# Kernel optimization log

Hardware: AMD Instinct MI355X
Metric: run time of the kernel (lower is better)

## Reference

```python
import jax, jax.numpy as jnp
import numpy as np

B = 131072
H_GAS = 8
H_EXT = 16
# gas order and net counts, total 99 tiny MLPs
GAS_SIZES = [23, 29, 13, 9, 3, 9, 13]  # h2o, h2o_sq, o3, co2, n2o, ch4, u
N_NETS = 29

# index maps taken verbatim from the 29 tau_gases assignment lines
H2O_ROWS = np.arange(23)
H2O_IDX = np.array([0,1,2,3,4,5,6,3,4,9,10,11,12,13,14,15,16,17,18,19,20,21,22])
O3_ROWS = np.array([0,1,2,17,18,19,20,21,22,25,26,27,28])
CO2_ROWS = np.array([0,1,2,5,6,9,10,13,14])
N2O_ROWS = np.array([0,1,2])
CH4_ROWS = np.array([0,1,2,3,4,7,8,11,12])
U_ROWS = np.array([0,1,2,15,16,17,18,19,20,21,22,27,28])


def setup_inputs() -> dict:
    key = jax.random.key(0)
    ks = jax.random.split(key, 23)
    f = jnp.float32
    inp = {
        'temp': jax.random.normal(ks[0], (B, 1), f),
        'pressure': jax.random.normal(ks[1], (B, 1), f),
        'comp_h2o': jax.random.uniform(ks[2], (B, 1), f),
        'comp_h2o_sq': jax.random.uniform(ks[3], (B, 1), f),
        'comp_o3': jax.random.uniform(ks[4], (B, 1), f),
        'comp_co2': jax.random.uniform(ks[5], (B, 1), f),
        'comp_n2o': jax.random.uniform(ks[6], (B, 1), f),
        'comp_ch4': jax.random.uniform(ks[7], (B, 1), f),
        'comp_u': jax.random.uniform(ks[8], (B, 1), f),
        'lwp': jax.random.uniform(ks[9], (B, 1), f, minval=0.05, maxval=1.0),
        'iwp': jax.random.uniform(ks[10], (B, 1), f, minval=0.05, maxval=1.0),
        'mu': jax.random.uniform(ks[11], (B, 1), f, minval=0.1, maxval=1.0),
        'mu_bar': jax.random.uniform(ks[12], (B, 1), f, minval=0.1, maxval=1.0),
        'gas_W1': jax.random.normal(ks[13], (99, 2, H_GAS), f) * 0.5,
        'gas_b1': jax.random.normal(ks[14], (99, H_GAS), f) * 0.1,
        'gas_W2': jax.random.normal(ks[15], (99, H_GAS, 1), f) * 0.5,
        'gas_b2': jax.random.uniform(ks[16], (99, 1), f, minval=0.05, maxval=0.5),
        'lw_w': jax.random.uniform(ks[17], (N_NETS, 1), f, minval=0.05, maxval=1.0),
        'iw_w': jax.random.uniform(ks[18], (N_NETS, 1), f, minval=0.05, maxval=1.0),
        'ext_W1': jax.random.normal(ks[19], (N_NETS, 4, H_EXT), f) * 0.5,
        'ext_b1': jax.random.normal(ks[20], (N_NETS, H_EXT), f) * 0.1,
        'ext_W2': jax.random.normal(ks[21], (N_NETS, H_EXT, 3), f) * 0.5,
        'ext_b2': jax.random.normal(ks[22], (N_NETS, 3), f) * 0.1,
    }
    return inp


def reference(temp, pressure, comp_h2o, comp_h2o_sq, comp_o3, comp_co2, comp_n2o,
              comp_ch4, comp_u, lwp, iwp, mu, mu_bar,
              gas_W1, gas_b1, gas_W2, gas_b2, lw_w, iw_w,
              ext_W1, ext_b1, ext_W2, ext_b2):
    b = temp.shape[0]
    X = jnp.concatenate([temp, pressure], axis=-1)              # [B,2]
    # all 99 per-gas tiny MLPs in one batched pass
    h = jax.nn.elu(jnp.einsum('bi,nih->nbh', X, gas_W1) + gas_b1[:, None, :])
    ke = jax.nn.relu(jnp.einsum('nbh,nho->nbo', h, gas_W2) + gas_b2[:, None, :])[..., 0]  # [99,B]
    comps = [comp_h2o, comp_h2o_sq, comp_o3, comp_co2, comp_n2o, comp_ch4, comp_u]
    comp_all = jnp.concatenate(
        [jnp.broadcast_to(c[:, 0][None, :], (n, b)) for c, n in zip(comps, GAS_SIZES)], axis=0)
    tau_all = ke * comp_all                                      # [99,B]
    h2o    = tau_all[0:23]
    h2o_sq = tau_all[23:52]
    o3     = tau_all[52:65]
    co2    = tau_all[65:74]
    n2o    = tau_all[74:77]
    ch4    = tau_all[77:86]
    u      = tau_all[86:99]
    # scatter-combine into the 29 spectral channels
    tau_g = h2o_sq                                               # every row has h2o_sq[k]
    tau_g = tau_g.at[H2O_ROWS].add(h2o[H2O_IDX])
    tau_g = tau_g.at[O3_ROWS].add(o3)
    tau_g = tau_g.at[CO2_ROWS].add(co2)
    tau_g = tau_g.at[N2O_ROWS].add(n2o)
    tau_g = tau_g.at[CH4_ROWS].add(ch4)
    tau_g = tau_g.at[U_ROWS].add(u)
    tau_lw = lw_w * lwp[:, 0][None, :]                           # [29,B]
    tau_iw = iw_w * iwp[:, 0][None, :]
    tau_total = tau_g + tau_lw + tau_iw
    in1 = tau_lw / tau_total
    in2 = tau_iw / tau_total
    mu_v, mub_v = mu[:, 0], mu_bar[:, 0]
    in3_dir = tau_total / mu_v[None, :]
    in3_dif = tau_total / mub_v[None, :]

    def ext(i1, i2, i3, m):
        Xe = jnp.stack([i1, i2, i3, jnp.broadcast_to(m[None, :], i1.shape)], axis=-1)  # [29,B,4]
        he = jax.nn.elu(jnp.einsum('nbi,nih->nbh', Xe, ext_W1) + ext_b1[:, None, :])
        return jax.nn.relu(jnp.einsum('nbh,nho->nbo', he, ext_W2) + ext_b2[:, None, :])

    e_direct = jax.nn.softmax(ext(in1, in2, in3_dir, mu_v), axis=-1)   # [29,B,3]
    e_diffuse = jax.nn.softmax(ext(in1, in2, in3_dif, mub_v), axis=-1)
    t_direct = jnp.exp(-in3_dir)
    t_diffuse = jnp.exp(-in3_dif)
    return (t_direct, t_diffuse, e_direct, e_diffuse)
```

## Files before the change

### kernel.cpp

```cpp
#include <hip/hip_runtime.h>
#include <math.h>

#define TPB 256
#define EPT 2

typedef float v2f __attribute__((ext_vector_type(2)));

#define VFMA(a, b, c) __builtin_elementwise_fma((a), (b), (c))
#define VMAX(a, b) __builtin_elementwise_max((a), (b))
#define LOG2E 1.4426950408889634f

struct f3 { float a, b, c; };

static __device__ __forceinline__ v2f sp(float s) { return (v2f){s, s}; }

static __device__ __forceinline__ float fexp2(float x) {
#if __has_builtin(__builtin_amdgcn_exp2f)
    return __builtin_amdgcn_exp2f(x);
#else
    return __expf(x * 0.6931471805599453f);
#endif
}

static __device__ __forceinline__ float fast_rcp(float x) {
    return __builtin_amdgcn_rcpf(x);
}

static __device__ __forceinline__ v2f elu2(v2f h) {
    v2f t = h * LOG2E;
    v2f e = {fexp2(t.x), fexp2(t.y)};
    e = e - 1.0f;
    return (v2f){h.x > 0.f ? h.x : e.x, h.y > 0.f ? h.y : e.y};
}

static __device__ const unsigned char NETS[29][8] = {
    {  0, 23,  52,  65,  74,  77,  86, 255},
    {  1, 24,  53,  66,  75,  78,  87, 255},
    {  2, 25,  54,  67,  76,  79,  88, 255},
    {  3, 26, 255, 255, 255,  80, 255, 255},
    {  4, 27, 255, 255, 255,  81, 255, 255},
    {  5, 28, 255,  68, 255, 255, 255, 255},
    {  6, 29, 255,  69, 255, 255, 255, 255},
    {  3, 30, 255, 255, 255,  82, 255, 255},
    {  4, 31, 255, 255, 255,  83, 255, 255},
    {  9, 32, 255,  70, 255, 255, 255, 255},
    { 10, 33, 255,  71, 255, 255, 255, 255},
    { 11, 34, 255, 255, 255,  84, 255, 255},
    { 12, 35, 255, 255, 255,  85, 255, 255},
    { 13, 36, 255,  72, 255, 255, 255, 255},
    { 14, 37, 255,  73, 255, 255, 255, 255},
    { 15, 38, 255, 255, 255, 255,  89, 255},
    { 16, 39, 255, 255, 255, 255,  90, 255},
    { 17, 40,  55, 255, 255, 255,  91, 255},
    { 18, 41,  56, 255, 255, 255,  92, 255},
    { 19, 42,  57, 255, 255, 255,  93, 255},
    { 20, 43,  58, 255, 255, 255,  94, 255},
    { 21, 44,  59, 255, 255, 255,  95, 255},
    { 22, 45,  60, 255, 255, 255,  96, 255},
    {255, 46, 255, 255, 255, 255, 255, 255},
    {255, 47, 255, 255, 255, 255, 255, 255},
    {255, 48,  61, 255, 255, 255, 255, 255},
    {255, 49,  62, 255, 255, 255, 255, 255},
    {255, 50,  63, 255, 255, 255,  97, 255},
    {255, 51,  64, 255, 255, 255,  98, 255}};

static __device__ __forceinline__ void softmax3_v2(v2f o0, v2f o1, v2f o2,
                                                   v2f& r0, v2f& r1, v2f& r2) {
    o0 = VMAX(o0, sp(0.f));
    o1 = VMAX(o1, sp(0.f));
    o2 = VMAX(o2, sp(0.f));
    v2f mx = VMAX(o0, VMAX(o1, o2));
    v2f nm = mx * (-LOG2E);
    v2f a0 = VFMA(o0, sp(LOG2E), nm);
    v2f a1 = VFMA(o1, sp(LOG2E), nm);
    v2f a2 = VFMA(o2, sp(LOG2E), nm);
    v2f e0 = {fexp2(a0.x), fexp2(a0.y)};
    v2f e1 = {fexp2(a1.x), fexp2(a1.y)};
    v2f e2 = {fexp2(a2.x), fexp2(a2.y)};
    v2f ssum = e0 + e1 + e2;
    v2f rs = {fast_rcp(ssum.x), fast_rcp(ssum.y)};
    r0 = e0 * rs; r1 = e1 * rs; r2 = e2 * rs;
}

template <bool GUARD>
__global__ __launch_bounds__(TPB, 5) void atm_kernel(
    const float* __restrict__ temp,
    const float* __restrict__ pressure,
    const float* __restrict__ c_h2o,
    const float* __restrict__ c_h2o_sq,
    const float* __restrict__ c_o3,
    const float* __restrict__ c_co2,
    const float* __restrict__ c_n2o,
    const float* __restrict__ c_ch4,
    const float* __restrict__ c_u,
    const float* __restrict__ lwp,
    const float* __restrict__ iwp,
    const float* __restrict__ mu,
    const float* __restrict__ mu_bar,
    const float* __restrict__ gW1,
    const float* __restrict__ gb1,
    const float* __restrict__ gW2,
    const float* __restrict__ gb2,
    const float* __restrict__ lw_w,
    const float* __restrict__ iw_w,
    const float* __restrict__ eW1,
    const float* __restrict__ eb1,
    const float* __restrict__ eW2,
    const float* __restrict__ eb2,
    float* __restrict__ out,
    int Bn)
{
    const int r = blockIdx.x;
    const int bA = blockIdx.y * (TPB * EPT) + threadIdx.x;
    if (GUARD && bA >= Bn) return;
    const int bB = bA + TPB;
    bool vB = true;
    int bBl = bB;
    if (GUARD) { vB = (bB < Bn); bBl = vB ? bB : bA; }

    const v2f t2  = {temp[bA],     temp[bBl]};
    const v2f p2  = {pressure[bA], pressure[bBl]};
    const v2f lwp2 = {lwp[bA],    lwp[bBl]};
    const v2f iwp2 = {iwp[bA],    iwp[bBl]};
    const v2f mu2  = {mu[bA],     mu[bBl]};
    const v2f mb2  = {mu_bar[bA], mu_bar[bBl]};

    v2f tg = sp(0.f);
    #pragma unroll
    for (int s = 0; s < 7; ++s) {
        const int n = NETS[r][s];
        if (n != 255) {
            const float* cp =
                (s == 0) ? c_h2o    : (s == 1) ? c_h2o_sq :
                (s == 2) ? c_o3     : (s == 3) ? c_co2    :
                (s == 4) ? c_n2o    : (s == 5) ? c_ch4    : c_u;
            const v2f cs = {cp[bA], cp[bBl]};
            const float4* W1 = (const float4*)(gW1 + (n << 4));
            const float4 wt0 = W1[0], wt1 = W1[1];
            const float4 wp0 = W1[2], wp1 = W1[3];
            const float4* B1 = (const float4*)(gb1 + (n << 3));
            const float4 bb0 = B1[0], bb1 = B1[1];
            const float4* W2 = (const float4*)(gW2 + (n << 3));
            const float4 wo0 = W2[0], wo1 = W2[1];
            v2f acc = sp(gb2[n]);
#define GAS_H(WT, WP, BB, WO, K)                                            \
            { v2f h = VFMA(t2, sp((WT).K), VFMA(p2, sp((WP).K), sp((BB).K))); \
              h = elu2(h);                                                   \
              acc = VFMA(h, sp((WO).K), acc); }
            GAS_H(wt0, wp0, bb0, wo0, x)
            GAS_H(wt0, wp0, bb0, wo0, y)
            GAS_H(wt0, wp0, bb0, wo0, z)
            GAS_H(wt0, wp0, bb0, wo0, w)
            GAS_H(wt1, wp1, bb1, wo1, x)
            GAS_H(wt1, wp1, bb1, wo1, y)
            GAS_H(wt1, wp1, bb1, wo1, z)
            GAS_H(wt1, wp1, bb1, wo1, w)
#undef GAS_H
            acc = VMAX(acc, sp(0.f));
            tg = VFMA(acc, cs, tg);
        }
    }

    const float lwr = lw_w[r], iwr = iw_w[r];
    v2f tlw = lwp2 * lwr;
    v2f tiw = iwp2 * iwr;
    v2f tt = tg + tlw + tiw;
    v2f rtt = {fast_rcp(tt.x), fast_rcp(tt.y)};
    v2f in1 = tlw * rtt;
    v2f in2 = tiw * rtt;
    v2f rmu = {fast_rcp(mu2.x), fast_rcp(mu2.y)};
    v2f rmb = {fast_rcp(mb2.x), fast_rcp(mb2.y)};
    v2f i3d = tt * rmu;
    v2f i3f = tt * rmb;

    const int idxA = r * Bn + bA;
    {
        v2f ad = i3d * (-LOG2E);
        v2f af = i3f * (-LOG2E);
        out[idxA] = fexp2(ad.x);
        out[29 * Bn + idxA] = fexp2(af.x);
        if (vB) {
            out[idxA + TPB] = fexp2(ad.y);
            out[29 * Bn + idxA + TPB] = fexp2(af.y);
        }
    }

    const float* w1  = eW1 + (r << 6);
    const float* ebv = eb1 + (r << 4);
    const float* w2  = eW2 + r * 48;
    const float bo0 = eb2[r * 3 + 0];
    const float bo1 = eb2[r * 3 + 1];
    const float bo2 = eb2[r * 3 + 2];

    v2f d0 = sp(bo0), d1 = sp(bo1), d2 = sp(bo2);
    v2f f0 = sp(bo0), f1 = sp(bo1), f2 = sp(bo2);

    #pragma unroll
    for (int q = 0; q < 4; ++q) {
        const float4 wA4 = *(const float4*)(w1 + 4 * q);
        const float4 wB4 = *(const float4*)(w1 + 16 + 4 * q);
        const float4 wC4 = *(const float4*)(w1 + 32 + 4 * q);
        const float4 wD4 = *(const float4*)(w1 + 48 + 4 * q);
        const float4 bj4 = *(const float4*)(ebv + 4 * q);
        const float4 u0  = *(const float4*)(w2 + 12 * q);
        const float4 u1  = *(const float4*)(w2 + 12 * q + 4);
        const float4 u2  = *(const float4*)(w2 + 12 * q + 8);
#define EXT_H(K, W20, W21, W22)                                               \
        { v2f bs = VFMA(in1, sp((wA4).K), VFMA(in2, sp((wB4).K), sp((bj4).K))); \
          v2f hd = elu2(VFMA(i3d, sp((wC4).K), VFMA(mu2, sp((wD4).K), bs)));   \
          v2f hf = elu2(VFMA(i3f, sp((wC4).K), VFMA(mb2, sp((wD4).K), bs)));   \
          d0 = VFMA(hd, sp(W20), d0); d1 = VFMA(hd, sp(W21), d1);              \
          d2 = VFMA(hd, sp(W22), d2);                                          \
          f0 = VFMA(hf, sp(W20), f0); f1 = VFMA(hf, sp(W21), f1);              \
          f2 = VFMA(hf, sp(W22), f2); }
        EXT_H(x, u0.x, u0.y, u0.z)
        EXT_H(y, u0.w, u1.x, u1.y)
        EXT_H(z, u1.z, u1.w, u2.x)
        EXT_H(w, u2.y, u2.z, u2.w)
#undef EXT_H
    }

    v2f r0, r1, r2;
    softmax3_v2(d0, d1, d2, r0, r1, r2);
    f3* pdA = (f3*)(out + 58 * Bn) + idxA;
    pdA[0] = (f3){r0.x, r1.x, r2.x};
    if (vB) pdA[TPB] = (f3){r0.y, r1.y, r2.y};
    softmax3_v2(f0, f1, f2, r0, r1, r2);
    f3* pfA = (f3*)(out + 145 * Bn) + idxA;
    pfA[0] = (f3){r0.x, r1.x, r2.x};
    if (vB) pfA[TPB] = (f3){r0.y, r1.y, r2.y};
}

extern "C" void kernel_launch(void* const* d_in, const int* in_sizes, int n_in,
                              void* d_out, int out_size, void* d_ws, size_t ws_size,
                              hipStream_t stream) {
    const int Bn = in_sizes[0];
    const int span = TPB * EPT;
    dim3 grid(29, (Bn + span - 1) / span);
    if (Bn % span == 0) {
        atm_kernel<false><<<grid, TPB, 0, stream>>>(
            (const float*)d_in[0],  (const float*)d_in[1],  (const float*)d_in[2],
            (const float*)d_in[3],  (const float*)d_in[4],  (const float*)d_in[5],
            (const float*)d_in[6],  (const float*)d_in[7],  (const float*)d_in[8],
            (const float*)d_in[9],  (const float*)d_in[10], (const float*)d_in[11],
            (const float*)d_in[12], (const float*)d_in[13], (const float*)d_in[14],
            (const float*)d_in[15], (const float*)d_in[16], (const float*)d_in[17],
            (const float*)d_in[18], (const float*)d_in[19], (const float*)d_in[20],
            (const float*)d_in[21], (const float*)d_in[22],
            (float*)d_out, Bn);
    } else {
        atm_kernel<true><<<grid, TPB, 0, stream>>>(
            (const float*)d_in[0],  (const float*)d_in[1],  (const float*)d_in[2],
            (const float*)d_in[3],  (const float*)d_in[4],  (const float*)d_in[5],
            (const float*)d_in[6],  (const float*)d_in[7],  (const float*)d_in[8],
            (const float*)d_in[9],  (const float*)d_in[10], (const float*)d_in[11],
            (const float*)d_in[12], (const float*)d_in[13], (const float*)d_in[14],
            (const float*)d_in[15], (const float*)d_in[16], (const float*)d_in[17],
            (const float*)d_in[18], (const float*)d_in[19], (const float*)d_in[20],
            (const float*)d_in[21], (const float*)d_in[22],
            (float*)d_out, Bn);
    }
}
```

Measured before the change: 210.5 us.

## Add grid-stride persistent kernel and branchless ELU, pack pointers in struct

Replaces the 2D grid of 29×256 blocks with a 1D grid-stride kernel capped near 2048 blocks, each looping over (row, batch-tile) items, when the batch tile count is a power of two. ELU is rewritten branchlessly as max(h,0)+exp(min(h,0))-1. Launch bounds drop the minimum-blocks hint of 5, which may change register allocation and occupancy. Kernel arguments are packed into a struct.

```diff
diff --git a/kernel.cpp b/kernel.cpp
--- a/kernel.cpp
+++ b/kernel.cpp
@@ -8,9 +8,21 @@
 
 #define VFMA(a, b, c) __builtin_elementwise_fma((a), (b), (c))
 #define VMAX(a, b) __builtin_elementwise_max((a), (b))
+#define VMIN(a, b) __builtin_elementwise_min((a), (b))
 #define LOG2E 1.4426950408889634f
 
 struct f3 { float a, b, c; };
+
+struct Ptrs {
+    const float *temp, *pressure;
+    const float *c0, *c1, *c2, *c3, *c4, *c5, *c6;
+    const float *lwp, *iwp, *mu, *mub;
+    const float *gW1, *gb1, *gW2, *gb2;
+    const float *lww, *iww;
+    const float *eW1, *eb1, *eW2, *eb2;
+    float* out;
+    int Bn;
+};
 
 static __device__ __forceinline__ v2f sp(float s) { return (v2f){s, s}; }
 
@@ -27,10 +39,9 @@
 }
 
 static __device__ __forceinline__ v2f elu2(v2f h) {
-    v2f t = h * LOG2E;
+    v2f t = VMIN(h, sp(0.f)) * LOG2E;
     v2f e = {fexp2(t.x), fexp2(t.y)};
-    e = e - 1.0f;
-    return (v2f){h.x > 0.f ? h.x : e.x, h.y > 0.f ? h.y : e.y};
+    return VMAX(h, sp(0.f)) + e - 1.0f;
 }
 
 static __device__ const unsigned char NETS[29][8] = {
@@ -83,47 +94,16 @@
 }
 
 template <bool GUARD>
-__global__ __launch_bounds__(TPB, 5) void atm_kernel(
-    const float* __restrict__ temp,
-    const float* __restrict__ pressure,
-    const float* __restrict__ c_h2o,
-    const float* __restrict__ c_h2o_sq,
-    const float* __restrict__ c_o3,
-    const float* __restrict__ c_co2,
-    const float* __restrict__ c_n2o,
-    const float* __restrict__ c_ch4,
-    const float* __restrict__ c_u,
-    const float* __restrict__ lwp,
-    const float* __restrict__ iwp,
-    const float* __restrict__ mu,
-    const float* __restrict__ mu_bar,
-    const float* __restrict__ gW1,
-    const float* __restrict__ gb1,
-    const float* __restrict__ gW2,
-    const float* __restrict__ gb2,
-    const float* __restrict__ lw_w,
-    const float* __restrict__ iw_w,
-    const float* __restrict__ eW1,
-    const float* __restrict__ eb1,
-    const float* __restrict__ eW2,
-    const float* __restrict__ eb2,
-    float* __restrict__ out,
-    int Bn)
-{
-    const int r = blockIdx.x;
-    const int bA = blockIdx.y * (TPB * EPT) + threadIdx.x;
-    if (GUARD && bA >= Bn) return;
-    const int bB = bA + TPB;
-    bool vB = true;
-    int bBl = bB;
-    if (GUARD) { vB = (bB < Bn); bBl = vB ? bB : bA; }
-
-    const v2f t2  = {temp[bA],     temp[bBl]};
-    const v2f p2  = {pressure[bA], pressure[bBl]};
-    const v2f lwp2 = {lwp[bA],    lwp[bBl]};
-    const v2f iwp2 = {iwp[bA],    iwp[bBl]};
-    const v2f mu2  = {mu[bA],     mu[bBl]};
-    const v2f mb2  = {mu_bar[bA], mu_bar[bBl]};
+static __device__ __forceinline__ void item_body(const Ptrs& P, int r, int bA,
+                                                 bool vB, int bBl) {
+    const int Bn = P.Bn;
+
+    const v2f t2  = {P.temp[bA],     P.temp[bBl]};
+    const v2f p2  = {P.pressure[bA], P.pressure[bBl]};
+    const v2f lwp2 = {P.lwp[bA], P.lwp[bBl]};
+    const v2f iwp2 = {P.iwp[bA], P.iwp[bBl]};
+    const v2f mu2  = {P.mu[bA],  P.mu[bBl]};
+    const v2f mb2  = {P.mub[bA], P.mub[bBl]};
 
     v2f tg = sp(0.f);
     #pragma unroll
@@ -131,18 +111,18 @@
         const int n = NETS[r][s];
         if (n != 255) {
             const float* cp =
-                (s == 0) ? c_h2o    : (s == 1) ? c_h2o_sq :
-                (s == 2) ? c_o3     : (s == 3) ? c_co2    :
-                (s == 4) ? c_n2o    : (s == 5) ? c_ch4    : c_u;
+                (s == 0) ? P.c0 : (s == 1) ? P.c1 :
+                (s == 2) ? P.c2 : (s == 3) ? P.c3 :
+                (s == 4) ? P.c4 : (s == 5) ? P.c5 : P.c6;
             const v2f cs = {cp[bA], cp[bBl]};
-            const float4* W1 = (const float4*)(gW1 + (n << 4));
+            const float4* W1 = (const float4*)(P.gW1 + (n << 4));
             const float4 wt0 = W1[0], wt1 = W1[1];
             const float4 wp0 = W1[2], wp1 = W1[3];
-            const float4* B1 = (const float4*)(gb1 + (n << 3));
+            const float4* B1 = (const float4*)(P.gb1 + (n << 3));
             const float4 bb0 = B1[0], bb1 = B1[1];
-            const float4* W2 = (const float4*)(gW2 + (n << 3));
+            const float4* W2 = (const float4*)(P.gW2 + (n << 3));
             const float4 wo0 = W2[0], wo1 = W2[1];
-            v2f acc = sp(gb2[n]);
+            v2f acc = sp(P.gb2[n]);
 #define GAS_H(WT, WP, BB, WO, K)                                            \
             { v2f h = VFMA(t2, sp((WT).K), VFMA(p2, sp((WP).K), sp((BB).K))); \
               h = elu2(h);                                                   \
@@ -161,7 +141,7 @@
         }
     }
 
-    const float lwr = lw_w[r], iwr = iw_w[r];
+    const float lwr = P.lww[r], iwr = P.iww[r];
     v2f tlw = lwp2 * lwr;
     v2f tiw = iwp2 * iwr;
     v2f tt = tg + tlw + tiw;
@@ -173,24 +153,25 @@
     v2f i3d = tt * rmu;
     v2f i3f = tt * rmb;
 
+    float* out = P.out;
     const int idxA = r * Bn + bA;
     {
         v2f ad = i3d * (-LOG2E);
         v2f af = i3f * (-LOG2E);
         out[idxA] = fexp2(ad.x);
         out[29 * Bn + idxA] = fexp2(af.x);
-        if (vB) {
+        if (!GUARD || vB) {
             out[idxA + TPB] = fexp2(ad.y);
             out[29 * Bn + idxA + TPB] = fexp2(af.y);
         }
     }
 
-    const float* w1  = eW1 + (r << 6);
-    const float* ebv = eb1 + (r << 4);
-    const float* w2  = eW2 + r * 48;
-    const float bo0 = eb2[r * 3 + 0];
-    const float bo1 = eb2[r * 3 + 1];
-    const float bo2 = eb2[r * 3 + 2];
+    const float* w1  = P.eW1 + (r << 6);
+    const float* ebv = P.eb1 + (r << 4);
+    const float* w2  = P.eW2 + r * 48;
+    const float bo0 = P.eb2[r * 3 + 0];
+    const float bo1 = P.eb2[r * 3 + 1];
+    const float bo2 = P.eb2[r * 3 + 2];
 
     v2f d0 = sp(bo0), d1 = sp(bo1), d2 = sp(bo2);
     v2f f0 = sp(bo0), f1 = sp(bo1), f2 = sp(bo2);
@@ -224,40 +205,71 @@
     softmax3_v2(d0, d1, d2, r0, r1, r2);
     f3* pdA = (f3*)(out + 58 * Bn) + idxA;
     pdA[0] = (f3){r0.x, r1.x, r2.x};
-    if (vB) pdA[TPB] = (f3){r0.y, r1.y, r2.y};
+    if (!GUARD || vB) pdA[TPB] = (f3){r0.y, r1.y, r2.y};
     softmax3_v2(f0, f1, f2, r0, r1, r2);
     f3* pfA = (f3*)(out + 145 * Bn) + idxA;
     pfA[0] = (f3){r0.x, r1.x, r2.x};
-    if (vB) pfA[TPB] = (f3){r0.y, r1.y, r2.y};
+    if (!GUARD || vB) pfA[TPB] = (f3){r0.y, r1.y, r2.y};
+}
+
+__global__ __launch_bounds__(TPB) void atm_persist(Ptrs P, int yshift,
+                                                   int items, int stride) {
+    const int ymask = (1 << yshift) - 1;
+    for (int it = blockIdx.x; it < items; it += stride) {
+        const int r = it >> yshift;
+        const int bA = ((it & ymask) * (TPB * EPT)) + threadIdx.x;
+        item_body<false>(P, r, bA, true, bA + TPB);
+    }
+}
+
+template <bool GUARD>
+__global__ __launch_bounds__(TPB) void atm_legacy(Ptrs P) {
+    const int r = blockIdx.x;
+    const int bA = blockIdx.y * (TPB * EPT) + threadIdx.x;
+    if (GUARD && bA >= P.Bn) return;
+    const int bB = bA + TPB;
+    bool vB = true;
+    int bBl = bB;
+    if (GUARD) { vB = (bB < P.Bn); bBl = vB ? bB : bA; }
+    item_body<GUARD>(P, r, bA, vB, bBl);
 }
 
 extern "C" void kernel_launch(void* const* d_in, const int* in_sizes, int n_in,
                               void* d_out, int out_size, void* d_ws, size_t ws_size,
                               hipStream_t stream) {
     const int Bn = in_sizes[0];
+    Ptrs P;
+    P.temp = (const float*)d_in[0];  P.pressure = (const float*)d_in[1];
+    P.c0 = (const float*)d_in[2];    P.c1 = (const float*)d_in[3];
+    P.c2 = (const float*)d_in[4];    P.c3 = (const float*)d_in[5];
+    P.c4 = (const float*)d_in[6];    P.c5 = (const float*)d_in[7];
+    P.c6 = (const float*)d_in[8];
+    P.lwp = (const float*)d_in[9];   P.iwp = (const float*)d_in[10];
+    P.mu = (const float*)d_in[11];   P.mub = (const float*)d_in[12];
+    P.gW1 = (const float*)d_in[13];  P.gb1 = (const float*)d_in[14];
+    P.gW2 = (const float*)d_in[15];  P.gb2 = (const float*)d_in[16];
+    P.lww = (const float*)d_in[17];  P.iww = (const float*)d_in[18];
+    P.eW1 = (const float*)d_in[19];  P.eb1 = (const float*)d_in[20];
+    P.eW2 = (const float*)d_in[21];  P.eb2 = (const float*)d_in[22];
+    P.out = (float*)d_out;
+    P.Bn = Bn;
+
     const int span = TPB * EPT;
-    dim3 grid(29, (Bn + span - 1) / span);
     if (Bn % span == 0) {
-        atm_kernel<false><<<grid, TPB, 0, stream>>>(
-            (const float*)d_in[0],  (const float*)d_in[1],  (const float*)d_in[2],
-            (const float*)d_in[3],  (const float*)d_in[4],  (const float*)d_in[5],
-            (const float*)d_in[6],  (const float*)d_in[7],  (const float*)d_in[8],
-            (const float*)d_in[9],  (const float*)d_in[10], (const float*)d_in[11],
-            (const float*)d_in[12], (const float*)d_in[13], (const float*)d_in[14],
-            (const float*)d_in[15], (const float*)d_in[16], (const float*)d_in[17],
-            (const float*)d_in[18], (const float*)d_in[19], (const float*)d_in[20],
-            (const float*)d_in[21], (const float*)d_in[22],
-            (float*)d_out, Bn);
-    } else {
-        atm_kernel<true><<<grid, TPB, 0, stream>>>(
-            (const float*)d_in[0],  (const float*)d_in[1],  (const float*)d_in[2],
-            (const float*)d_in[3],  (const float*)d_in[4],  (const float*)d_in[5],
-            (const float*)d_in[6],  (const float*)d_in[7],  (const float*)d_in[8],
-            (const float*)d_in[9],  (const float*)d_in[10], (const float*)d_in[11],
-            (const float*)d_in[12], (const float*)d_in[13], (const float*)d_in[14],
-            (const float*)d_in[15], (const float*)d_in[16], (const float*)d_in[17],
-            (const float*)d_in[18], (const float*)d_in[19], (const float*)d_in[20],
-            (const float*)d_in[21], (const float*)d_in[22],
-            (float*)d_out, Bn);
-    }
-}
+        const int yc = Bn / span;
+        if ((yc & (yc - 1)) == 0) {
+            int yshift = 0;
+            while ((1 << yshift) != yc) ++yshift;
+            const int items = 29 * yc;
+            const int iters = (items + 2047) / 2048;
+            const int grid  = (items + iters - 1) / iters;
+            atm_persist<<<grid, TPB, 0, stream>>>(P, yshift, items, grid);
+            return;
+        }
+        dim3 g(29, yc);
+        atm_legacy<false><<<g, TPB, 0, stream>>>(P);
+        return;
+    }
+    dim3 g(29, (Bn + span - 1) / span);
+    atm_legacy<true><<<g, TPB, 0, stream>>>(P);
+}
```

Measured after the change: 222.7 us. 5.8% more time.
